# Kernel optimization log

Hardware: AMD Instinct MI355X
Metric: run time of the kernel (lower is better)

The kernel has to match this reference:

```python
import jax, jax.numpy as jnp
import numpy as np

N_NODES = 50000
N_EDGES = 600000
DIM = 128
HEADS = 8
HEAD_DIM = DIM // HEADS  # 16


def leaky(x, slope=0.01):
    return jnp.where(x >= 0, x, slope * x)


def gat_layer(x, W, a_src, a_dst, bias, src, dst):
    # x: [N, DIM]; W: [DIM, DIM]; a_src/a_dst: [HEADS, HEAD_DIM]; bias: [DIM]
    N = x.shape[0]
    xh = (x @ W).reshape(N, HEADS, HEAD_DIM)
    alpha_src = jnp.sum(xh * a_src, axis=-1)  # [N, H]
    alpha_dst = jnp.sum(xh * a_dst, axis=-1)  # [N, H]
    e = leaky(alpha_src[src] + alpha_dst[dst], 0.2)  # [E, H], PyG negative_slope=0.2
    # segment softmax over edges sharing the same destination node
    e_max = jax.ops.segment_max(e, dst, num_segments=N)
    ex = jnp.exp(e - e_max[dst])
    denom = jax.ops.segment_sum(ex, dst, num_segments=N)
    alpha = ex / (denom[dst] + 1e-16)
    out = jax.ops.segment_sum(xh[src] * alpha[:, :, None], dst, num_segments=N)
    return out.reshape(N, DIM) + bias


def setup_inputs() -> dict:
    key = jax.random.key(0)
    ks = jax.random.split(key, 20)
    s_d = 1.0 / np.sqrt(DIM)
    s_h = 1.0 / np.sqrt(DIM // 2)
    inp = {
        'features': jax.random.normal(ks[0], (N_NODES, DIM), jnp.float32),
        'edge_index': jax.random.randint(ks[1], (2, N_EDGES), 0, N_NODES, jnp.int64)
            if jax.config.jax_enable_x64 else
            jax.random.randint(ks[1], (2, N_EDGES), 0, N_NODES).astype(jnp.int32),
        'W1': jax.random.normal(ks[2], (DIM, DIM), jnp.float32) * s_d,
        'a_src1': jax.random.normal(ks[3], (HEADS, HEAD_DIM), jnp.float32) * s_d,
        'a_dst1': jax.random.normal(ks[4], (HEADS, HEAD_DIM), jnp.float32) * s_d,
        'b1': jnp.zeros((DIM,), jnp.float32),
        'W2': jax.random.normal(ks[5], (DIM, DIM), jnp.float32) * s_d,
        'a_src2': jax.random.normal(ks[6], (HEADS, HEAD_DIM), jnp.float32) * s_d,
        'a_dst2': jax.random.normal(ks[7], (HEADS, HEAD_DIM), jnp.float32) * s_d,
        'b2': jnp.zeros((DIM,), jnp.float32),
        'wm1': jax.random.normal(ks[8], (DIM, DIM // 2), jnp.float32) * s_d,
        'bm1': jnp.zeros((DIM // 2,), jnp.float32),
        'wm2': jax.random.normal(ks[9], (DIM // 2, 1), jnp.float32) * s_h,
        'bm2': jnp.zeros((1,), jnp.float32),
        'wa1': jax.random.normal(ks[10], (DIM, DIM // 2), jnp.float32) * s_d,
        'ba1': jnp.zeros((DIM // 2,), jnp.float32),
        'wa2': jax.random.normal(ks[11], (DIM // 2, DIM), jnp.float32) * s_h,
        'ba2': jnp.zeros((DIM,), jnp.float32),
        'gamma': jnp.ones((DIM,), jnp.float32),
        'beta': jnp.zeros((DIM,), jnp.float32),
    }
    return inp


def reference(features, edge_index, W1, a_src1, a_dst1, b1, W2, a_src2, a_dst2, b2,
              wm1, bm1, wm2, bm2, wa1, ba1, wa2, ba2, gamma, beta):
    N = features.shape[0]
    loops = jnp.arange(N, dtype=edge_index.dtype)
    src = jnp.concatenate([edge_index[0], loops])  # PyG add_self_loops=True
    dst = jnp.concatenate([edge_index[1], loops])
    h = leaky(gat_layer(features, W1, a_src1, a_dst1, b1, src, dst))
    h = leaky(gat_layer(h, W2, a_src2, a_dst2, b2, src, dst))
    scores = (leaky(h @ wm1 + bm1) @ wm2 + bm2)[:, 0]  # [N]
    w = jax.nn.softmax(scores, axis=0)
    agg = jnp.sum(w[:, None] * h, axis=0)  # [DIM]
    z = leaky(agg @ wa1 + ba1) @ wa2 + ba2
    mu = jnp.mean(z)
    var = jnp.mean((z - mu) ** 2)
    return gamma * (z - mu) / jnp.sqrt(var + 1e-5) + beta
```

## Files before the change

kernel.cpp:

```cpp
#include <hip/hip_runtime.h>
#include <math.h>

#define DIM 128
#define HEADS 8
#define HD 16
#define CAP 64

typedef __attribute__((ext_vector_type(8))) short s16x8;
typedef __attribute__((ext_vector_type(8))) unsigned short u16x8;
typedef __attribute__((ext_vector_type(4))) float f32x4;

__device__ __forceinline__ float lrelu(float x, float s) { return x >= 0.f ? x : s * x; }

__device__ __forceinline__ unsigned short f2bf(float x) {
  unsigned u = __float_as_uint(x);
  return (unsigned short)((u + 0x7FFFu + ((u >> 16) & 1u)) >> 16);
}
__device__ __forceinline__ float bf2f(unsigned short b) {
  return __uint_as_float(((unsigned)b) << 16);
}

__global__ __launch_bounds__(256) void k_scan_blk(const int* __restrict__ cnt, int n,
                                                  int* __restrict__ excl, int* __restrict__ bsum) {
  __shared__ int wsum[4];
  int tid = threadIdx.x, l = tid & 63, w = tid >> 6;
  int i = blockIdx.x * 256 + tid;
  int v = (i < n) ? cnt[i] : 0;
  int s = v;
#pragma unroll
  for (int off = 1; off < 64; off <<= 1) {
    int t = __shfl_up(s, off, 64);
    if (l >= off) s += t;
  }
  if (l == 63) wsum[w] = s;
  __syncthreads();
  int add = 0;
#pragma unroll
  for (int k = 0; k < 4; ++k) add += (k < w) ? wsum[k] : 0;
  if (i < n) excl[i] = s + add - v;
  if (tid == 255) bsum[blockIdx.x] = s + add;
}

__global__ __launch_bounds__(256) void k_scan_top(const int* __restrict__ bsum, int nb,
                                                  int* __restrict__ boff, int* __restrict__ rowptrN) {
  __shared__ int wsum[4];
  int tid = threadIdx.x, l = tid & 63, w = tid >> 6;
  int v = (tid < nb) ? bsum[tid] : 0;
  int s = v;
#pragma unroll
  for (int off = 1; off < 64; off <<= 1) {
    int t = __shfl_up(s, off, 64);
    if (l >= off) s += t;
  }
  if (l == 63) wsum[w] = s;
  __syncthreads();
  int add = 0;
#pragma unroll
  for (int k = 0; k < 4; ++k) add += (k < w) ? wsum[k] : 0;
  if (tid < nb) boff[tid] = s + add - v;
  if (tid == 255) *rowptrN = s + add;
}

__global__ __launch_bounds__(256) void k_scan_fix(int* __restrict__ cursor, const int* __restrict__ boff,
                                                  int n, int* __restrict__ rowptr) {
  int i = blockIdx.x * 256 + threadIdx.x;
  if (i < n) {
    int r = boff[blockIdx.x] + cursor[i];
    rowptr[i] = r;
    cursor[i] = r;
  }
}

__global__ void k_scatter(const int* __restrict__ ei, int E, int N,
                          int* __restrict__ cursor, int* __restrict__ colb) {
  int tot = E + N;
  for (int i = blockIdx.x * blockDim.x + threadIdx.x; i < tot; i += gridDim.x * blockDim.x) {
    int s, d;
    if (i < E) { s = ei[i]; d = ei[E + i]; } else { s = i - E; d = s; }
    int pos = atomicAdd(&cursor[d], 1);
    colb[pos] = s;
  }
}

__global__ __launch_bounds__(256) void k_prep(
    const float* __restrict__ W1, const float* __restrict__ as1, const float* __restrict__ ad1,
    const float* __restrict__ W2, const float* __restrict__ as2, const float* __restrict__ ad2,
    const float* __restrict__ wm1,
    unsigned short* __restrict__ wh1,
    unsigned short* __restrict__ sh1, unsigned short* __restrict__ sl1,
    unsigned short* __restrict__ wh2,
    unsigned short* __restrict__ sh2, unsigned short* __restrict__ sl2,
    unsigned short* __restrict__ mh, unsigned short* __restrict__ ml,
    int* __restrict__ cnt, int N) {
  int b = blockIdx.x, tid = threadIdx.x;
  if (b < 32) {
    int layer = b >> 4;
    const float* W = layer ? W2 : W1;
    unsigned short* wh = layer ? wh2 : wh1;
    int lo = (b & 15) * 1024;
    for (int idx = lo + tid; idx < lo + 1024; idx += 256) {
      int n = idx >> 7, k = idx & 127;
      wh[idx] = f2bf(W[k * DIM + n]);
    }
  } else if (b < 36) {
    int layer = (b - 32) >> 1;
    const float* W = layer ? W2 : W1;
    const float* avs = layer ? as2 : as1;
    const float* avd = layer ? ad2 : ad1;
    unsigned short* sh = layer ? sh2 : sh1;
    unsigned short* sl = layer ? sl2 : sl1;
    int lo = ((b - 32) & 1) * 1024;
    for (int idx = lo + tid; idx < lo + 1024; idx += 256) {
      int n = idx >> 7, k = idx & 127;
      float acc = 0.f;
      if (n < 8) {
#pragma unroll
        for (int j = 0; j < 16; ++j) acc += W[k * DIM + n * 16 + j] * avs[n * 16 + j];
      } else {
        int h = n - 8;
#pragma unroll
        for (int j = 0; j < 16; ++j) acc += W[k * DIM + h * 16 + j] * avd[h * 16 + j];
      }
      unsigned short hb = f2bf(acc);
      sh[idx] = hb;
      sl[idx] = f2bf(acc - bf2f(hb));
    }
  } else if (b < 44) {
    int lo = (b - 36) * 1024;
    for (int idx = lo + tid; idx < lo + 1024; idx += 256) {
      int j = idx >> 7, k = idx & 127;
      float v = wm1[k * 64 + j];
      unsigned short hb = f2bf(v);
      mh[idx] = hb;
      ml[idx] = f2bf(v - bf2f(hb));
    }
  } else {
    int i0 = (b - 44) * 2048 + tid * 8;
    if (i0 + 8 <= N) {
      int4 z = {0, 0, 0, 0};
      *(int4*)(cnt + i0) = z;
      *(int4*)(cnt + i0 + 4) = z;
    } else {
      for (int i = i0; i < N; ++i) cnt[i] = 0;
    }
  }
}

template <int BF16IN, int FUSEHIST>
__global__ __launch_bounds__(256) void k_linear_mfma(
    const void* __restrict__ xin,
    const unsigned short* __restrict__ wh,
    const unsigned short* __restrict__ sh, const unsigned short* __restrict__ sl,
    unsigned short* __restrict__ xhb, float* __restrict__ asrc, float* __restrict__ adst,
    int N, int nrt, int GL,
    const int* __restrict__ ei, int E, int* __restrict__ cnt) {
  if constexpr (FUSEHIST) {
    if ((int)blockIdx.x >= GL) {
      int tot = E + N;
      int nhb = gridDim.x - GL;
      for (int i = ((int)blockIdx.x - GL) * 256 + (int)threadIdx.x; i < tot; i += nhb * 256) {
        int d = (i < E) ? ei[E + i] : (i - E);
        atomicAdd(&cnt[d], 1);
      }
      return;
    }
  }
  int tid = threadIdx.x, l = tid & 63, w = tid >> 6;
  int g = l >> 4, c = l & 15;
  int t0 = w * 2, t1 = w * 2 + 1;
  int stride = FUSEHIST ? GL : (int)gridDim.x;

  const s16x8* Bh = (const s16x8*)wh;
  const s16x8* Shp = (const s16x8*)sh;
  const s16x8* Slp = (const s16x8*)sl;
  s16x8 B0[4], B1[4], S0[4], S1[4];
#pragma unroll
  for (int kt = 0; kt < 4; ++kt) {
    B0[kt] = Bh[(t0 * 16 + c) * 16 + kt * 4 + g];
    B1[kt] = Bh[(t1 * 16 + c) * 16 + kt * 4 + g];
    S0[kt] = Shp[c * 16 + kt * 4 + g];
    S1[kt] = Slp[c * 16 + kt * 4 + g];
  }

  for (int rt = blockIdx.x; rt < nrt; rt += stride) {
    int rbase = rt * 16;
    int rc = min(rbase + c, N - 1);
    s16x8 A[4];
    if constexpr (BF16IN) {
      const s16x8* xr = (const s16x8*)((const unsigned short*)xin + (size_t)rc * DIM);
#pragma unroll
      for (int kt = 0; kt < 4; ++kt) A[kt] = xr[kt * 4 + g];
    } else {
      const float4* xf = (const float4*)((const float*)xin + (size_t)rc * DIM);
#pragma unroll
      for (int kt = 0; kt < 4; ++kt) {
        float4 p = xf[kt * 8 + g * 2];
        float4 q = xf[kt * 8 + g * 2 + 1];
        s16x8 a;
        a[0] = (short)f2bf(p.x); a[1] = (short)f2bf(p.y);
        a[2] = (short)f2bf(p.z); a[3] = (short)f2bf(p.w);
        a[4] = (short)f2bf(q.x); a[5] = (short)f2bf(q.y);
        a[6] = (short)f2bf(q.z); a[7] = (short)f2bf(q.w);
        A[kt] = a;
      }
    }
    f32x4 acc0 = {0.f, 0.f, 0.f, 0.f}, acc1 = {0.f, 0.f, 0.f, 0.f};
#pragma unroll
    for (int kt = 0; kt < 4; ++kt) {
      acc0 = __builtin_amdgcn_mfma_f32_16x16x32_bf16(A[kt], B0[kt], acc0, 0, 0, 0);
      acc1 = __builtin_amdgcn_mfma_f32_16x16x32_bf16(A[kt], B1[kt], acc1, 0, 0, 0);
    }
#pragma unroll
    for (int r = 0; r < 4; ++r) {
      int rr = rbase + g * 4 + r;
      if (rr < N) {
        xhb[(size_t)rr * DIM + t0 * 16 + c] = f2bf(acc0[r]);
        xhb[(size_t)rr * DIM + t1 * 16 + c] = f2bf(acc1[r]);
      }
    }
    if (w == 0) {
      f32x4 accS = {0.f, 0.f, 0.f, 0.f};
#pragma unroll
      for (int kt = 0; kt < 4; ++kt) {
        accS = __builtin_amdgcn_mfma_f32_16x16x32_bf16(A[kt], S0[kt], accS, 0, 0, 0);
        accS = __builtin_amdgcn_mfma_f32_16x16x32_bf16(A[kt], S1[kt], accS, 0, 0, 0);
      }
#pragma unroll
      for (int r = 0; r < 4; ++r) {
        int rr = rbase + g * 4 + r;
        if (rr < N) {
          if (c < 8) asrc[rr * HEADS + c] = accS[r];
          else adst[rr * HEADS + (c - 8)] = accS[r];
        }
      }
    }
  }
}

__global__ __launch_bounds__(256) void k_gat_agg(const int* __restrict__ rowptr, const int* __restrict__ colb,
                                                 const unsigned short* __restrict__ xhb,
                                                 const float* __restrict__ asrc, const float* __restrict__ adst,
                                                 const float* __restrict__ bias,
                                                 unsigned short* __restrict__ houtb, int N) {
  __shared__ int ci[4][CAP];
  int tid = threadIdx.x, lane = tid & 63, wv = tid >> 6;
  int n = blockIdx.x * 4 + wv;
  int base = 0, deg = 0;
  if (n < N) { base = rowptr[n]; deg = rowptr[n + 1] - base; }
  if (lane < deg && lane < CAP) ci[wv][lane] = colb[base + lane];
  __syncthreads();
  if (n >= N) return;

  int qt = lane >> 4, q = lane & 15;
  int h = q >> 1;
  float adn = adst[n * HEADS + h];
  float den = 0.f;
  float a0 = 0.f, a1 = 0.f, a2 = 0.f, a3 = 0.f, a4 = 0.f, a5 = 0.f, a6 = 0.f, a7 = 0.f;
#define EDGE(ii) { \
    int c_ = ((ii) < CAP) ? ci[wv][(ii)] : colb[base + (ii)]; \
    float e_ = lrelu(asrc[c_ * HEADS + h] + adn, 0.2f); \
    float w_ = __expf(e_); \
    den += w_; \
    u16x8 u_ = *(const u16x8*)(xhb + (size_t)c_ * DIM + q * 8); \
    a0 = fmaf(w_, bf2f((unsigned short)u_[0]), a0); \
    a1 = fmaf(w_, bf2f((unsigned short)u_[1]), a1); \
    a2 = fmaf(w_, bf2f((unsigned short)u_[2]), a2); \
    a3 = fmaf(w_, bf2f((unsigned short)u_[3]), a3); \
    a4 = fmaf(w_, bf2f((unsigned short)u_[4]), a4); \
    a5 = fmaf(w_, bf2f((unsigned short)u_[5]), a5); \
    a6 = fmaf(w_, bf2f((unsigned short)u_[6]), a6); \
    a7 = fmaf(w_, bf2f((unsigned short)u_[7]), a7); }
  int i = qt;
  for (; i + 4 < deg; i += 8) { EDGE(i); EDGE(i + 4); }
  for (; i < deg; i += 4) { EDGE(i); }
#undef EDGE
  den += __shfl_xor(den, 16, 64); den += __shfl_xor(den, 32, 64);
  a0 += __shfl_xor(a0, 16, 64); a0 += __shfl_xor(a0, 32, 64);
  a1 += __shfl_xor(a1, 16, 64); a1 += __shfl_xor(a1, 32, 64);
  a2 += __shfl_xor(a2, 16, 64); a2 += __shfl_xor(a2, 32, 64);
  a3 += __shfl_xor(a3, 16, 64); a3 += __shfl_xor(a3, 32, 64);
  a4 += __shfl_xor(a4, 16, 64); a4 += __shfl_xor(a4, 32, 64);
  a5 += __shfl_xor(a5, 16, 64); a5 += __shfl_xor(a5, 32, 64);
  a6 += __shfl_xor(a6, 16, 64); a6 += __shfl_xor(a6, 32, 64);
  a7 += __shfl_xor(a7, 16, 64); a7 += __shfl_xor(a7, 32, 64);
  if (qt == 0) {
    float r = 1.f / (den + 1e-16f);
    const float4* bp = (const float4*)(bias + q * 8);
    float4 b0 = bp[0], b1 = bp[1];
    u16x8 o;
    o[0] = f2bf(lrelu(fmaf(a0, r, b0.x), 0.01f));
    o[1] = f2bf(lrelu(fmaf(a1, r, b0.y), 0.01f));
    o[2] = f2bf(lrelu(fmaf(a2, r, b0.z), 0.01f));
    o[3] = f2bf(lrelu(fmaf(a3, r, b0.w), 0.01f));
    o[4] = f2bf(lrelu(fmaf(a4, r, b1.x), 0.01f));
    o[5] = f2bf(lrelu(fmaf(a5, r, b1.y), 0.01f));
    o[6] = f2bf(lrelu(fmaf(a6, r, b1.z), 0.01f));
    o[7] = f2bf(lrelu(fmaf(a7, r, b1.w), 0.01f));
    *(u16x8*)(houtb + (size_t)n * DIM + q * 8) = o;
  }
}

__global__ __launch_bounds__(256) void k_score_pool(
    const unsigned short* __restrict__ h2b,
    const unsigned short* __restrict__ mh, const unsigned short* __restrict__ ml,
    const float* __restrict__ bm1, const float* __restrict__ wm2, const float* __restrict__ bm2,
    float* __restrict__ pagg, float* __restrict__ psum, int N) {
  __shared__ float se[4][16];
  __shared__ float blkacc[4][128];
  __shared__ float swave[4];
  int tid = threadIdx.x, l = tid & 63, w = tid >> 6;
  int g = l >> 4, c = l & 15;
  int rbase = blockIdx.x * 64 + w * 16;
  int rc = min(rbase + c, N - 1);
  const s16x8* xr = (const s16x8*)(h2b + (size_t)rc * DIM);
  s16x8 A[4];
#pragma unroll
  for (int kt = 0; kt < 4; ++kt) A[kt] = xr[kt * 4 + g];

  const s16x8* Bh = (const s16x8*)mh;
  const s16x8* Bl = (const s16x8*)ml;
  float v[4] = {0.f, 0.f, 0.f, 0.f};
#pragma unroll
  for (int ct = 0; ct < 4; ++ct) {
    f32x4 acc = {0.f, 0.f, 0.f, 0.f};
#pragma unroll
    for (int kt = 0; kt < 4; ++kt) {
      s16x8 bh = Bh[(ct * 16 + c) * 16 + kt * 4 + g];
      s16x8 bl = Bl[(ct * 16 + c) * 16 + kt * 4 + g];
      acc = __builtin_amdgcn_mfma_f32_16x16x32_bf16(A[kt], bh, acc, 0, 0, 0);
      acc = __builtin_amdgcn_mfma_f32_16x16x32_bf16(A[kt], bl, acc, 0, 0, 0);
    }
    int col = ct * 16 + c;
    float b = bm1[col], w2 = wm2[col];
#pragma unroll
    for (int r = 0; r < 4; ++r) v[r] += lrelu(acc[r] + b, 0.01f) * w2;
  }
#pragma unroll
  for (int r = 0; r < 4; ++r) {
    v[r] += __shfl_xor(v[r], 1, 64);
    v[r] += __shfl_xor(v[r], 2, 64);
    v[r] += __shfl_xor(v[r], 4, 64);
    v[r] += __shfl_xor(v[r], 8, 64);
  }
  float b2 = bm2[0];
  float e[4];
#pragma unroll
  for (int r = 0; r < 4; ++r) {
    int rr = rbase + g * 4 + r;
    e[r] = (rr < N) ? __expf(v[r] + b2) : 0.f;
  }
  if (c == 0) {
#pragma unroll
    for (int r = 0; r < 4; ++r) se[w][g * 4 + r] = e[r];
  }
  __syncthreads();
  float emy = se[w][c];
  float pa[32];
#pragma unroll
  for (int kt = 0; kt < 4; ++kt)
#pragma unroll
    for (int j = 0; j < 8; ++j)
      pa[kt * 8 + j] = emy * bf2f((unsigned short)A[kt][j]);
#pragma unroll
  for (int k = 0; k < 32; ++k) {
    pa[k] += __shfl_xor(pa[k], 1, 64);
    pa[k] += __shfl_xor(pa[k], 2, 64);
    pa[k] += __shfl_xor(pa[k], 4, 64);
    pa[k] += __shfl_xor(pa[k], 8, 64);
  }
  if (c == 0) {
#pragma unroll
    for (int kt = 0; kt < 4; ++kt)
#pragma unroll
      for (int j = 0; j < 8; ++j)
        blkacc[w][kt * 32 + g * 8 + j] = pa[kt * 8 + j];
  }
  float ws = e[0] + e[1] + e[2] + e[3];
  ws += __shfl_xor(ws, 16, 64);
  ws += __shfl_xor(ws, 32, 64);
  if (l == 0) swave[w] = ws;
  __syncthreads();
  if (tid < 128) {
    float s = blkacc[0][tid] + blkacc[1][tid] + blkacc[2][tid] + blkacc[3][tid];
    pagg[(size_t)blockIdx.x * DIM + tid] = s;
  }
  if (tid == 0) psum[blockIdx.x] = swave[0] + swave[1] + swave[2] + swave[3];
}

__global__ __launch_bounds__(1024) void k_final(const float* __restrict__ psum, const float* __restrict__ pagg,
                                                int nb,
                                                const float* __restrict__ wa1, const float* __restrict__ ba1,
                                                const float* __restrict__ wa2, const float* __restrict__ ba2,
                                                const float* __restrict__ gamma, const float* __restrict__ beta,
                                                float* __restrict__ out) {
  __shared__ float redz[1024];
  __shared__ float reda[8][128];
  __shared__ float sa[128], shh[64], red[128];
  int t = threadIdx.x;
  float zp = 0.f;
  for (int b = t; b < nb; b += 1024) zp += psum[b];
  redz[t] = zp;
  __syncthreads();
  for (int st = 512; st > 0; st >>= 1) { if (t < st) redz[t] += redz[t + st]; __syncthreads(); }
  int d = t & 127, g = t >> 7;
  float ag = 0.f;
  for (int b = g; b < nb; b += 8) ag += pagg[(size_t)b * DIM + d];
  reda[g][d] = ag;
  __syncthreads();
  if (g == 0) {
    float s = 0.f;
#pragma unroll
    for (int k = 0; k < 8; ++k) s += reda[k][d];
    sa[d] = s / redz[0];
  }
  __syncthreads();
  if (t < 64) {
    float a = 0.f;
    for (int k = 0; k < 128; ++k) a = fmaf(sa[k], wa1[k * 64 + t], a);
    a += ba1[t];
    shh[t] = lrelu(a, 0.01f);
  }
  __syncthreads();
  float zval = 0.f;
  if (t < 128) {
    zval = ba2[t];
    for (int j = 0; j < 64; ++j) zval = fmaf(shh[j], wa2[j * 128 + t], zval);
    red[t] = zval;
  }
  __syncthreads();
  for (int st = 64; st > 0; st >>= 1) { if (t < st) red[t] += red[t + st]; __syncthreads(); }
  float mu = red[0] / 128.f;
  __syncthreads();
  if (t < 128) red[t] = (zval - mu) * (zval - mu);
  __syncthreads();
  for (int st = 64; st > 0; st >>= 1) { if (t < st) red[t] += red[t + st]; __syncthreads(); }
  float var = red[0] / 128.f;
  if (t < 128) out[t] = gamma[t] * (zval - mu) / sqrtf(var + 1e-5f) + beta[t];
}

extern "C" void kernel_launch(void* const* d_in, const int* in_sizes, int n_in,
                              void* d_out, int out_size, void* d_ws, size_t ws_size,
                              hipStream_t stream) {
  const float* feat = (const float*)d_in[0];
  const int* ei = (const int*)d_in[1];
  const float* W1 = (const float*)d_in[2];
  const float* as1 = (const float*)d_in[3];
  const float* ad1 = (const float*)d_in[4];
  const float* b1 = (const float*)d_in[5];
  const float* W2 = (const float*)d_in[6];
  const float* as2 = (const float*)d_in[7];
  const float* ad2 = (const float*)d_in[8];
  const float* b2 = (const float*)d_in[9];
  const float* wm1 = (const float*)d_in[10];
  const float* bm1 = (const float*)d_in[11];
  const float* wm2 = (const float*)d_in[12];
  const float* bm2 = (const float*)d_in[13];
  const float* wa1 = (const float*)d_in[14];
  const float* ba1 = (const float*)d_in[15];
  const float* wa2 = (const float*)d_in[16];
  const float* ba2 = (const float*)d_in[17];
  const float* gamma = (const float*)d_in[18];
  const float* beta = (const float*)d_in[19];
  float* out = (float*)d_out;

  int N = in_sizes[0] / DIM;
  int E = in_sizes[1] / 2;
  int NB = (N + 255) / 256;
  int nrt = (N + 15) / 16;
  int ZB = (N + 2047) / 2048;
  int GL = 1024;
  int GH = 512;
  int gs = (N + 63) / 64;

  char* ws = (char*)d_ws;
  size_t off = 0;
  auto alloc = [&](size_t bytes) -> void* {
    void* p = ws + off;
    off = (off + bytes + 255) & ~(size_t)255;
    return p;
  };
  int* cnt = (int*)alloc((size_t)N * 4);
  int* rowptr = (int*)alloc((size_t)(N + 1) * 4);
  int* cursor = (int*)alloc((size_t)N * 4);
  int* colb = (int*)alloc((size_t)(E + N) * 4);
  unsigned short* xhb = (unsigned short*)alloc((size_t)N * DIM * 2);
  unsigned short* h1b = (unsigned short*)alloc((size_t)N * DIM * 2);
  unsigned short* h2b = (unsigned short*)alloc((size_t)N * DIM * 2);
  float* asrcb = (float*)alloc((size_t)N * HEADS * 4);
  float* adstb = (float*)alloc((size_t)N * HEADS * 4);
  float* pagg = (float*)alloc((size_t)gs * DIM * 4);
  float* psum = (float*)alloc((size_t)gs * 4);
  int* bsum = (int*)alloc((size_t)NB * 4);
  int* boff = (int*)alloc((size_t)NB * 4);
  unsigned short* wh1 = (unsigned short*)alloc(DIM * DIM * 2);
  unsigned short* sh1 = (unsigned short*)alloc(16 * DIM * 2);
  unsigned short* sl1 = (unsigned short*)alloc(16 * DIM * 2);
  unsigned short* wh2 = (unsigned short*)alloc(DIM * DIM * 2);
  unsigned short* sh2 = (unsigned short*)alloc(16 * DIM * 2);
  unsigned short* sl2 = (unsigned short*)alloc(16 * DIM * 2);
  unsigned short* mh = (unsigned short*)alloc(64 * DIM * 2);
  unsigned short* ml = (unsigned short*)alloc(64 * DIM * 2);

  k_prep<<<44 + ZB, 256, 0, stream>>>(W1, as1, ad1, W2, as2, ad2, wm1,
                                      wh1, sh1, sl1, wh2, sh2, sl2, mh, ml, cnt, N);

  k_linear_mfma<0, 1><<<GL + GH, 256, 0, stream>>>(feat, wh1, sh1, sl1, xhb, asrcb, adstb,
                                                   N, nrt, GL, ei, E, cnt);

  k_scan_blk<<<NB, 256, 0, stream>>>(cnt, N, cursor, bsum);
  k_scan_top<<<1, 256, 0, stream>>>(bsum, NB, boff, rowptr + N);
  k_scan_fix<<<NB, 256, 0, stream>>>(cursor, boff, N, rowptr);
  k_scatter<<<1024, 256, 0, stream>>>(ei, E, N, cursor, colb);

  int ga = (N + 3) / 4;
  k_gat_agg<<<ga, 256, 0, stream>>>(rowptr, colb, xhb, asrcb, adstb, b1, h1b, N);
  k_linear_mfma<1, 0><<<1024, 256, 0, stream>>>(h1b, wh2, sh2, sl2, xhb, asrcb, adstb,
                                                N, nrt, 0, nullptr, 0, nullptr);
  k_gat_agg<<<ga, 256, 0, stream>>>(rowptr, colb, xhb, asrcb, adstb, b2, h2b, N);

  k_score_pool<<<gs, 256, 0, stream>>>(h2b, mh, ml, bm1, wm2, bm2, pagg, psum, N);
  k_final<<<1, 1024, 0, stream>>>(psum, pagg, gs, wa1, ba1, wa2, ba2, gamma, beta, out);
}
```

Measured before the change: 235.0 us.

## Stage linear outputs through LDS for coalesced stores and prefetch next row tile

The MFMA linear kernel now writes its bf16 results and attention scalars into shared-memory tiles, then stores them to global memory as 16-byte vectors per thread instead of scattered 2-byte stores. It also software-prefetches the next row tile's A operand before the store phase so loads overlap with writeback. Grid sizes for the linear blocks and histogram blocks are retuned. This adds two block barriers per tile and some LDS usage, which may reduce occupancy.

```diff
diff --git a/kernel.cpp b/kernel.cpp
--- a/kernel.cpp
+++ b/kernel.cpp
@@ -165,6 +165,8 @@
       return;
     }
   }
+  __shared__ unsigned short tile[16][136];
+  __shared__ float atile[16][16];
   int tid = threadIdx.x, l = tid & 63, w = tid >> 6;
   int g = l >> 4, c = l & 15;
   int t0 = w * 2, t1 = w * 2 + 1;
@@ -182,10 +184,8 @@
     S1[kt] = Slp[c * 16 + kt * 4 + g];
   }
 
-  for (int rt = blockIdx.x; rt < nrt; rt += stride) {
-    int rbase = rt * 16;
-    int rc = min(rbase + c, N - 1);
-    s16x8 A[4];
+  auto loadA = [&](int rt, s16x8* A) {
+    int rc = min(rt * 16 + c, N - 1);
     if constexpr (BF16IN) {
       const s16x8* xr = (const s16x8*)((const unsigned short*)xin + (size_t)rc * DIM);
 #pragma unroll
@@ -204,36 +204,57 @@
         A[kt] = a;
       }
     }
+  };
+
+  int rt = blockIdx.x;
+  if (rt >= nrt) return;
+  s16x8 A[4];
+  loadA(rt, A);
+  for (;;) {
     f32x4 acc0 = {0.f, 0.f, 0.f, 0.f}, acc1 = {0.f, 0.f, 0.f, 0.f};
 #pragma unroll
     for (int kt = 0; kt < 4; ++kt) {
       acc0 = __builtin_amdgcn_mfma_f32_16x16x32_bf16(A[kt], B0[kt], acc0, 0, 0, 0);
       acc1 = __builtin_amdgcn_mfma_f32_16x16x32_bf16(A[kt], B1[kt], acc1, 0, 0, 0);
     }
-#pragma unroll
-    for (int r = 0; r < 4; ++r) {
-      int rr = rbase + g * 4 + r;
-      if (rr < N) {
-        xhb[(size_t)rr * DIM + t0 * 16 + c] = f2bf(acc0[r]);
-        xhb[(size_t)rr * DIM + t1 * 16 + c] = f2bf(acc1[r]);
-      }
-    }
+    f32x4 accS = {0.f, 0.f, 0.f, 0.f};
     if (w == 0) {
-      f32x4 accS = {0.f, 0.f, 0.f, 0.f};
 #pragma unroll
       for (int kt = 0; kt < 4; ++kt) {
         accS = __builtin_amdgcn_mfma_f32_16x16x32_bf16(A[kt], S0[kt], accS, 0, 0, 0);
         accS = __builtin_amdgcn_mfma_f32_16x16x32_bf16(A[kt], S1[kt], accS, 0, 0, 0);
       }
-#pragma unroll
-      for (int r = 0; r < 4; ++r) {
-        int rr = rbase + g * 4 + r;
-        if (rr < N) {
-          if (c < 8) asrc[rr * HEADS + c] = accS[r];
-          else adst[rr * HEADS + (c - 8)] = accS[r];
-        }
+    }
+    int rtn = rt + stride;
+    bool more = rtn < nrt;
+    s16x8 An[4];
+    if (more) loadA(rtn, An);
+#pragma unroll
+    for (int r = 0; r < 4; ++r) {
+      tile[g * 4 + r][t0 * 16 + c] = f2bf(acc0[r]);
+      tile[g * 4 + r][t1 * 16 + c] = f2bf(acc1[r]);
+    }
+    if (w == 0) {
+#pragma unroll
+      for (int r = 0; r < 4; ++r) atile[g * 4 + r][c] = accS[r];
+    }
+    __syncthreads();
+    {
+      int row = tid >> 4, cb = tid & 15;
+      int rr = rt * 16 + row;
+      if (rr < N) {
+        u16x8 v = *(const u16x8*)&tile[row][cb * 8];
+        *(u16x8*)(xhb + (size_t)rr * DIM + cb * 8) = v;
+        float av = atile[row][cb];
+        if (cb < 8) asrc[rr * HEADS + cb] = av;
+        else adst[rr * HEADS + (cb - 8)] = av;
       }
     }
+    if (!more) break;
+    __syncthreads();
+#pragma unroll
+    for (int kt = 0; kt < 4; ++kt) A[kt] = An[kt];
+    rt = rtn;
   }
 }
 
@@ -468,8 +489,8 @@
   int NB = (N + 255) / 256;
   int nrt = (N + 15) / 16;
   int ZB = (N + 2047) / 2048;
-  int GL = 1024;
-  int GH = 512;
+  int GL = 1280;
+  int GH = 448;
   int gs = (N + 63) / 64;
 
   char* ws = (char*)d_ws;
@@ -514,8 +535,8 @@
 
   int ga = (N + 3) / 4;
   k_gat_agg<<<ga, 256, 0, stream>>>(rowptr, colb, xhb, asrcb, adstb, b1, h1b, N);
-  k_linear_mfma<1, 0><<<1024, 256, 0, stream>>>(h1b, wh2, sh2, sl2, xhb, asrcb, adstb,
-                                                N, nrt, 0, nullptr, 0, nullptr);
+  k_linear_mfma<1, 0><<<GL, 256, 0, stream>>>(h1b, wh2, sh2, sl2, xhb, asrcb, adstb,
+                                              N, nrt, 0, nullptr, 0, nullptr);
   k_gat_agg<<<ga, 256, 0, stream>>>(rowptr, colb, xhb, asrcb, adstb, b2, h2b, N);
 
   k_score_pool<<<gs, 256, 0, stream>>>(h2b, mh, ml, bm1, wm2, bm2, pagg, psum, N);
```

New measurement: 239.3 us. About the same (+1.8%).

## Tile linear MFMA kernel to 64 rows per block with LDS-staged coalesced stores

Applied to the files above, without the earlier changes.

The linear projection kernel changes from a grid-stride loop over 16-row tiles, where each wave redundantly loaded the same A rows, to one block per 64 rows. Each wave now handles 2 output column tiles across 4 row groups, and the attention-score MFMA work is spread over all four waves instead of only wave 0. Results go through shared memory and are written back as 16-byte vector stores rather than scattered 2-byte stores. The cost is more registers per thread for A fragments and accumulators, plus a block-wide barrier. The launch also moves from a fixed 1024 blocks to one block per 64 rows, and the histogram block count changes.

```diff
diff --git a/kernel.cpp b/kernel.cpp
--- a/kernel.cpp
+++ b/kernel.cpp
@@ -152,7 +152,7 @@
     const unsigned short* __restrict__ wh,
     const unsigned short* __restrict__ sh, const unsigned short* __restrict__ sl,
     unsigned short* __restrict__ xhb, float* __restrict__ asrc, float* __restrict__ adst,
-    int N, int nrt, int GL,
+    int N, int GL,
     const int* __restrict__ ei, int E, int* __restrict__ cnt) {
   if constexpr (FUSEHIST) {
     if ((int)blockIdx.x >= GL) {
@@ -165,10 +165,12 @@
       return;
     }
   }
+  __shared__ unsigned short tile[64][136];
+  __shared__ float atile[64][16];
   int tid = threadIdx.x, l = tid & 63, w = tid >> 6;
   int g = l >> 4, c = l & 15;
-  int t0 = w * 2, t1 = w * 2 + 1;
-  int stride = FUSEHIST ? GL : (int)gridDim.x;
+  int t0 = w * 2, t1 = t0 + 1;
+  int rb = blockIdx.x * 64;
 
   const s16x8* Bh = (const s16x8*)wh;
   const s16x8* Shp = (const s16x8*)sh;
@@ -182,57 +184,71 @@
     S1[kt] = Slp[c * 16 + kt * 4 + g];
   }
 
-  for (int rt = blockIdx.x; rt < nrt; rt += stride) {
-    int rbase = rt * 16;
-    int rc = min(rbase + c, N - 1);
-    s16x8 A[4];
+  s16x8 A[4][4];
+#pragma unroll
+  for (int q = 0; q < 4; ++q) {
+    int rc = min(rb + q * 16 + c, N - 1);
     if constexpr (BF16IN) {
       const s16x8* xr = (const s16x8*)((const unsigned short*)xin + (size_t)rc * DIM);
 #pragma unroll
-      for (int kt = 0; kt < 4; ++kt) A[kt] = xr[kt * 4 + g];
+      for (int kt = 0; kt < 4; ++kt) A[q][kt] = xr[kt * 4 + g];
     } else {
       const float4* xf = (const float4*)((const float*)xin + (size_t)rc * DIM);
 #pragma unroll
       for (int kt = 0; kt < 4; ++kt) {
         float4 p = xf[kt * 8 + g * 2];
-        float4 q = xf[kt * 8 + g * 2 + 1];
+        float4 qq = xf[kt * 8 + g * 2 + 1];
         s16x8 a;
         a[0] = (short)f2bf(p.x); a[1] = (short)f2bf(p.y);
         a[2] = (short)f2bf(p.z); a[3] = (short)f2bf(p.w);
-        a[4] = (short)f2bf(q.x); a[5] = (short)f2bf(q.y);
-        a[6] = (short)f2bf(q.z); a[7] = (short)f2bf(q.w);
-        A[kt] = a;
+        a[4] = (short)f2bf(qq.x); a[5] = (short)f2bf(qq.y);
+        a[6] = (short)f2bf(qq.z); a[7] = (short)f2bf(qq.w);
+        A[q][kt] = a;
       }
     }
-    f32x4 acc0 = {0.f, 0.f, 0.f, 0.f}, acc1 = {0.f, 0.f, 0.f, 0.f};
-#pragma unroll
-    for (int kt = 0; kt < 4; ++kt) {
-      acc0 = __builtin_amdgcn_mfma_f32_16x16x32_bf16(A[kt], B0[kt], acc0, 0, 0, 0);
-      acc1 = __builtin_amdgcn_mfma_f32_16x16x32_bf16(A[kt], B1[kt], acc1, 0, 0, 0);
-    }
+  }
+
+  f32x4 acc[4][2];
+#pragma unroll
+  for (int q = 0; q < 4; ++q) {
+    acc[q][0] = (f32x4){0.f, 0.f, 0.f, 0.f};
+    acc[q][1] = (f32x4){0.f, 0.f, 0.f, 0.f};
+  }
+#pragma unroll
+  for (int kt = 0; kt < 4; ++kt)
+#pragma unroll
+    for (int q = 0; q < 4; ++q) {
+      acc[q][0] = __builtin_amdgcn_mfma_f32_16x16x32_bf16(A[q][kt], B0[kt], acc[q][0], 0, 0, 0);
+      acc[q][1] = __builtin_amdgcn_mfma_f32_16x16x32_bf16(A[q][kt], B1[kt], acc[q][1], 0, 0, 0);
+    }
+  f32x4 accS = {0.f, 0.f, 0.f, 0.f};
+#pragma unroll
+  for (int kt = 0; kt < 4; ++kt) {
+    accS = __builtin_amdgcn_mfma_f32_16x16x32_bf16(A[w][kt], S0[kt], accS, 0, 0, 0);
+    accS = __builtin_amdgcn_mfma_f32_16x16x32_bf16(A[w][kt], S1[kt], accS, 0, 0, 0);
+  }
+
+#pragma unroll
+  for (int q = 0; q < 4; ++q)
 #pragma unroll
     for (int r = 0; r < 4; ++r) {
-      int rr = rbase + g * 4 + r;
-      if (rr < N) {
-        xhb[(size_t)rr * DIM + t0 * 16 + c] = f2bf(acc0[r]);
-        xhb[(size_t)rr * DIM + t1 * 16 + c] = f2bf(acc1[r]);
-      }
-    }
-    if (w == 0) {
-      f32x4 accS = {0.f, 0.f, 0.f, 0.f};
-#pragma unroll
-      for (int kt = 0; kt < 4; ++kt) {
-        accS = __builtin_amdgcn_mfma_f32_16x16x32_bf16(A[kt], S0[kt], accS, 0, 0, 0);
-        accS = __builtin_amdgcn_mfma_f32_16x16x32_bf16(A[kt], S1[kt], accS, 0, 0, 0);
-      }
-#pragma unroll
-      for (int r = 0; r < 4; ++r) {
-        int rr = rbase + g * 4 + r;
-        if (rr < N) {
-          if (c < 8) asrc[rr * HEADS + c] = accS[r];
-          else adst[rr * HEADS + (c - 8)] = accS[r];
-        }
-      }
+      tile[q * 16 + g * 4 + r][t0 * 16 + c] = f2bf(acc[q][0][r]);
+      tile[q * 16 + g * 4 + r][t1 * 16 + c] = f2bf(acc[q][1][r]);
+    }
+#pragma unroll
+  for (int r = 0; r < 4; ++r) atile[w * 16 + g * 4 + r][c] = accS[r];
+  __syncthreads();
+
+#pragma unroll
+  for (int p = 0; p < 4; ++p) {
+    int row = p * 16 + (tid >> 4), cb = tid & 15;
+    int rr = rb + row;
+    if (rr < N) {
+      u16x8 v = *(const u16x8*)&tile[row][cb * 8];
+      *(u16x8*)(xhb + (size_t)rr * DIM + cb * 8) = v;
+      float av = atile[row][cb];
+      if (cb < 8) asrc[rr * HEADS + cb] = av;
+      else adst[rr * HEADS + (cb - 8)] = av;
     }
   }
 }
@@ -466,10 +482,9 @@
   int N = in_sizes[0] / DIM;
   int E = in_sizes[1] / 2;
   int NB = (N + 255) / 256;
-  int nrt = (N + 15) / 16;
   int ZB = (N + 2047) / 2048;
-  int GL = 1024;
-  int GH = 512;
+  int GL = (N + 63) / 64;
+  int GH = 448;
   int gs = (N + 63) / 64;
 
   char* ws = (char*)d_ws;
@@ -505,7 +520,7 @@
                                       wh1, sh1, sl1, wh2, sh2, sl2, mh, ml, cnt, N);
 
   k_linear_mfma<0, 1><<<GL + GH, 256, 0, stream>>>(feat, wh1, sh1, sl1, xhb, asrcb, adstb,
-                                                   N, nrt, GL, ei, E, cnt);
+                                                   N, GL, ei, E, cnt);
 
   k_scan_blk<<<NB, 256, 0, stream>>>(cnt, N, cursor, bsum);
   k_scan_top<<<1, 256, 0, stream>>>(bsum, NB, boff, rowptr + N);
@@ -514,8 +529,8 @@
 
   int ga = (N + 3) / 4;
   k_gat_agg<<<ga, 256, 0, stream>>>(rowptr, colb, xhb, asrcb, adstb, b1, h1b, N);
-  k_linear_mfma<1, 0><<<1024, 256, 0, stream>>>(h1b, wh2, sh2, sl2, xhb, asrcb, adstb,
-                                                N, nrt, 0, nullptr, 0, nullptr);
+  k_linear_mfma<1, 0><<<GL, 256, 0, stream>>>(h1b, wh2, sh2, sl2, xhb, asrcb, adstb,
+                                              N, GL, nullptr, 0, nullptr);
   k_gat_agg<<<ga, 256, 0, stream>>>(rowptr, colb, xhb, asrcb, adstb, b2, h2b, N);
 
   k_score_pool<<<gs, 256, 0, stream>>>(h2b, mh, ml, bm1, wm2, bm2, pagg, psum, N);
```

New measurement: 243.7 us. +3.7%, slower.
